# Optimization experiments

Measured on AMD Instinct MI355X. Metric: run time of the kernel, lower is better.

## Reference

```python
import jax, jax.numpy as jnp
import numpy as np

N = 16      # num_nodes
D = 128     # embedding_dim
H = 8       # num_heads
F = 512     # feedforward_dim
L = 4       # num_layers
IN = 64     # per-node input dim (joint_pos 32 + joint_vel 32)
B = 16384   # batch


def _ln(x, g, b):
    m = x.mean(-1, keepdims=True)
    v = ((x - m) ** 2).mean(-1, keepdims=True)
    return (x - m) * jax.lax.rsqrt(v + 1e-5) * g + b


def setup_inputs() -> dict:
    key = jax.random.key(0)
    ks = jax.random.split(key, 24)
    s = 0.02
    inp = {
        'joint_pos': jax.random.normal(ks[0], (B, 32), jnp.float32),
        'joint_vel': jax.random.normal(ks[1], (B, 32), jnp.float32),
        'adjacency': jax.random.randint(ks[2], (N, N), 0, 2).astype(jnp.int32),
        # per-node embedder (distinct Linear per node, stacked)
        'embed_W': jax.random.normal(ks[3], (N, IN, D), jnp.float32) * s,
        'embed_b': jnp.zeros((N, D), jnp.float32),
        'pos_emb': jax.random.normal(ks[4], (N, D), jnp.float32) * s,
        # per-layer attention params, stacked over layer dim
        'Wq': jax.random.normal(ks[5], (L, D, D), jnp.float32) * s,
        'bq': jnp.zeros((L, D), jnp.float32),
        'Wk': jax.random.normal(ks[6], (L, D, D), jnp.float32) * s,
        'bk': jnp.zeros((L, D), jnp.float32),
        'Wv': jax.random.normal(ks[7], (L, D, D), jnp.float32) * s,
        'bv': jnp.zeros((L, D), jnp.float32),
        'Wo': jax.random.normal(ks[8], (L, D, D), jnp.float32) * s,
        'bo': jnp.zeros((L, D), jnp.float32),
        'ln1_g': jnp.ones((L, D), jnp.float32),
        'ln1_b': jnp.zeros((L, D), jnp.float32),
        'ln2_g': jnp.ones((L, D), jnp.float32),
        'ln2_b': jnp.zeros((L, D), jnp.float32),
        'W1': jax.random.normal(ks[9], (L, D, F), jnp.float32) * s,
        'b1': jnp.zeros((L, F), jnp.float32),
        'W2': jax.random.normal(ks[10], (L, F, D), jnp.float32) * s,
        'b2': jnp.zeros((L, D), jnp.float32),
    }
    return inp


def reference(joint_pos, joint_vel, adjacency, embed_W, embed_b, pos_emb,
              Wq, bq, Wk, bk, Wv, bv, Wo, bo,
              ln1_g, ln1_b, ln2_g, ln2_b, W1, b1, W2, b2):
    # adjacency with forced self-loops -> additive attention mask [N, N]
    adj = adjacency.astype(bool) | jnp.eye(N, dtype=bool)
    mask = jnp.where(adj, 0.0, -jnp.inf).astype(jnp.float32)

    # every node sees the full concatenated obs (list-variant obs_node_dict)
    feats = jnp.concatenate([joint_pos, joint_vel], axis=-1)        # [B, IN]
    # distinct per-node linear embedders, batched as one einsum
    x = jnp.einsum('bi,nio->bno', feats, embed_W) + embed_b + pos_emb  # [B, N, D]

    dh = D // H
    scale = 1.0 / (dh ** 0.5)
    for l in range(L):  # BoT-Hard: mask on every layer; pre-LN
        h = _ln(x, ln1_g[l], ln1_b[l])
        q = (h @ Wq[l] + bq[l]).reshape(-1, N, H, dh)
        k = (h @ Wk[l] + bk[l]).reshape(-1, N, H, dh)
        v = (h @ Wv[l] + bv[l]).reshape(-1, N, H, dh)
        s = jnp.einsum('bnhd,bmhd->bhnm', q, k) * scale + mask       # [B, H, N, N]
        a = jax.nn.softmax(s, axis=-1)
        o = jnp.einsum('bhnm,bmhd->bnhd', a, v).reshape(-1, N, D)
        x = x + o @ Wo[l] + bo[l]
        h2 = _ln(x, ln2_g[l], ln2_b[l])
        x = x + jax.nn.relu(h2 @ W1[l] + b1[l]) @ W2[l] + b2[l]
    return x
```

## Files before the change

### kernel.cpp

```cpp
#include <hip/hip_runtime.h>
#include <stdint.h>

typedef __bf16 bf16;
typedef bf16 bf16x8 __attribute__((ext_vector_type(8)));
typedef bf16 bf16x4 __attribute__((ext_vector_type(4)));
typedef float f32x4 __attribute__((ext_vector_type(4)));
typedef uint32_t u32;
typedef uint8_t u8;

#define B_TOT 16384
#define SWG 8
#define NWGS (B_TOT / SWG)

__device__ __forceinline__ f32x4 mfma32(bf16x8 a, bf16x8 b, f32x4 c) {
  return __builtin_amdgcn_mfma_f32_16x16x32_bf16(a, b, c, 0, 0, 0);
}
__device__ __forceinline__ bf16x8 zero8() {
  bf16x8 v;
#pragma unroll
  for (int j = 0; j < 8; j++) v[j] = (bf16)0.f;
  return v;
}

__device__ __forceinline__ void lds_fence() {
  __builtin_amdgcn_sched_barrier(0);
  asm volatile("s_waitcnt lgkmcnt(0)" ::: "memory");
  __builtin_amdgcn_sched_barrier(0);
}

__device__ __forceinline__ void bar_lg() {
  __builtin_amdgcn_sched_barrier(0);
  asm volatile("s_waitcnt lgkmcnt(0)" ::: "memory");
  __builtin_amdgcn_s_barrier();
  __builtin_amdgcn_sched_barrier(0);
}
__device__ __forceinline__ void bar_v0() {
  __builtin_amdgcn_sched_barrier(0);
  asm volatile("s_waitcnt vmcnt(0) lgkmcnt(0)" ::: "memory");
  __builtin_amdgcn_s_barrier();
  __builtin_amdgcn_sched_barrier(0);
}
__device__ __forceinline__ void bar_v2() {
  __builtin_amdgcn_sched_barrier(0);
  asm volatile("s_waitcnt vmcnt(2) lgkmcnt(0)" ::: "memory");
  __builtin_amdgcn_s_barrier();
  __builtin_amdgcn_sched_barrier(0);
}

__device__ __forceinline__ void stage16(const u8* __restrict__ src, int rowstride, int colbase,
                                        u8* dst, int tid) {
  __builtin_amdgcn_sched_barrier(0);
#pragma unroll
  for (int rr = 0; rr < 2; ++rr) {
    u32 o = (u32)(rr * 512 + tid) * 16u;
    u32 row = o >> 7, cb = o & 0x7Fu;
    const u8* s = src + (size_t)row * (size_t)rowstride + (size_t)colbase
                      + (size_t)(cb ^ ((row & 7u) << 4));
    __builtin_amdgcn_global_load_lds((const __attribute__((address_space(1))) u32*)s,
                                     (__attribute__((address_space(3))) u32*)(dst + o),
                                     16, 0, 0);
  }
}

__device__ __forceinline__ void st_row(u8* base, int row, int col, bf16 v) {
  *(bf16*)(base + (u32)(row * 256) + (u32)((2 * col) ^ ((row & 7) << 4))) = v;
}

__device__ __forceinline__ void loadA_rm(const u8* R, int g, int c, bf16x8 a[2][4]) {
  const u32 sw = (u32)(c & 7) << 4;
#pragma unroll
  for (int mt = 0; mt < 2; ++mt)
#pragma unroll
    for (int ks = 0; ks < 4; ++ks)
      a[mt][ks] = *(const bf16x8*)(R + (u32)((mt * 16 + c) * 256)
                                     + (((u32)(ks * 64 + g * 16)) ^ sw));
}

__device__ __forceinline__ void gemm_half(const u8* Wb, int khalf, const bf16x8 a[2][4],
                                          f32x4 acc[2][4], int nh, int g, int c) {
  const u32 sw = (u32)(c & 7) << 4;
#pragma unroll
  for (int ksl = 0; ksl < 2; ++ksl) {
    int ks = khalf * 2 + ksl;
#pragma unroll
    for (int nt = 0; nt < 4; ++nt) {
      bf16x8 b = *(const bf16x8*)(Wb + (u32)((nh * 64 + nt * 16 + c) * 128)
                                     + (((u32)(ksl * 64 + g * 16)) ^ sw));
      acc[0][nt] = mfma32(a[0][ks], b, acc[0][nt]);
      acc[1][nt] = mfma32(a[1][ks], b, acc[1][nt]);
    }
  }
}

template <bool RELU>
__device__ __forceinline__ void epi_rm(const f32x4 acc[2][4], const float* __restrict__ bias,
                                       u8* Rdst, int nh, int g, int c) {
#pragma unroll
  for (int nt = 0; nt < 4; ++nt) {
    int col = nh * 64 + nt * 16 + c;
    float bb = bias[col];
#pragma unroll
    for (int mt = 0; mt < 2; ++mt)
#pragma unroll
      for (int r = 0; r < 4; ++r) {
        float v = acc[mt][nt][r] + bb;
        if (RELU) v = fmaxf(v, 0.f);
        st_row(Rdst, mt * 16 + 4 * g + r, col, (bf16)v);
      }
  }
}

__device__ __forceinline__ void ln_part(const f32x4 x[2][4], float sS[2][4], float sS2[2][4]) {
#pragma unroll
  for (int mt = 0; mt < 2; ++mt) {
    f32x4 a = {0.f, 0.f, 0.f, 0.f}, b = {0.f, 0.f, 0.f, 0.f};
#pragma unroll
    for (int nt = 0; nt < 4; ++nt) { a += x[mt][nt]; b += x[mt][nt] * x[mt][nt]; }
#pragma unroll
    for (int r = 0; r < 4; ++r) {
      float s = a[r], s2 = b[r];
#pragma unroll
      for (int off = 1; off < 16; off <<= 1) { s += __shfl_xor(s, off); s2 += __shfl_xor(s2, off); }
      sS[mt][r] = s; sS2[mt][r] = s2;
    }
  }
}

__global__ void __launch_bounds__(512, 2)
bot_main(const int* __restrict__ adj,
         const float* __restrict__ embB, const float* __restrict__ posE,
         const float* __restrict__ pbq, const float* __restrict__ pbk,
         const float* __restrict__ pbv, const float* __restrict__ pbo,
         const float* __restrict__ l1g, const float* __restrict__ l1b,
         const float* __restrict__ l2g, const float* __restrict__ l2b,
         const float* __restrict__ pb1, const float* __restrict__ pb2,
         const bf16* __restrict__ feats, const bf16* __restrict__ embWT,
         const bf16* __restrict__ wqT, const bf16* __restrict__ wkT,
         const bf16* __restrict__ wvT, const bf16* __restrict__ woT,
         const bf16* __restrict__ w1T, const bf16* __restrict__ w2T,
         float* __restrict__ out) {
  __shared__ u8 smem[163840];
  const int tid = threadIdx.x;
  const int w = tid >> 6, lane = tid & 63, g = lane >> 4, c = lane & 15;
  const int p = w >> 1, nh = w & 1;
  const int S0 = blockIdx.x * SWG;
  const u32 sw = (u32)(c & 7) << 4;

  u8* pairb = smem + p * 24576;
  u8* RA = pairb;
  u8* Rq = pairb + 8192;
  u8* Rk = pairb + 16384;
  u8* WB0 = smem + 98304;
  u8* WB1 = smem + 114688;
  u8* WB2 = smem + 131072;
  u8* WB3 = smem + 147456;
  float* scr = (float*)Rk;

  float maskr[4];
#pragma unroll
  for (int r = 0; r < 4; ++r) {
    int n = 4 * g + r;
    maskr[r] = (adj[n * 16 + c] != 0 || n == c) ? 0.f : -1e9f;
  }

  {
    float* x0 = (float*)smem;
    f32x4 ea[16] = {};
    bf16x8 af[2];
#pragma unroll
    for (int ks = 0; ks < 2; ++ks)
      af[ks] = *(const bf16x8*)(feats + (size_t)(S0 + (c & 7)) * 64 + ks * 32 + g * 8);
#pragma unroll
    for (int nt = 0; nt < 16; ++nt) {
#pragma unroll
      for (int ks = 0; ks < 2; ++ks) {
        bf16x8 bw = *(const bf16x8*)(embWT + (size_t)(w * 256 + nt * 16 + c) * 64 + ks * 32 + g * 8);
        ea[nt] = mfma32(af[ks], bw, ea[nt]);
      }
    }
    if (g < 2) {
#pragma unroll
      for (int nt = 0; nt < 16; ++nt)
#pragma unroll
        for (int r = 0; r < 4; ++r)
          x0[(4 * g + r) * 2048 + w * 256 + nt * 16 + c] = ea[nt][r];
    }
  }
  __syncthreads();

  f32x4 x[2][4];
  {
    const float* x0 = (const float*)smem;
#pragma unroll
    for (int nt = 0; nt < 4; ++nt)
#pragma unroll
      for (int r = 0; r < 4; ++r) {
        int n = 4 * g + r, d = nh * 64 + nt * 16 + c;
        float eb = embB[n * 128 + d] + posE[n * 128 + d];
#pragma unroll
        for (int mt = 0; mt < 2; ++mt)
          x[mt][nt][r] = x0[(2 * p + mt) * 2048 + n * 128 + d] + eb;
      }
  }
  __syncthreads();

  bf16x8 Ah[2][4], Ah2[2][4], Au[2][4];

#pragma unroll 1
  for (int l = 0; l < 4; ++l) {
    const u8* Wq_l = (const u8*)(wqT + (size_t)l * 16384);
    const u8* Wk_l = (const u8*)(wkT + (size_t)l * 16384);
    const u8* Wv_l = (const u8*)(wvT + (size_t)l * 16384);
    const u8* Wo_l = (const u8*)(woT + (size_t)l * 16384);
    const u8* W1_l = (const u8*)(w1T + (size_t)l * 65536);
    const u8* W2_l = (const u8*)(w2T + (size_t)l * 65536);

    float sS[2][4], sS2[2][4], mean[2][4], rstd[2][4];

    ln_part(x, sS, sS2);
    if (c == 0) {
#pragma unroll
      for (int mt = 0; mt < 2; ++mt)
#pragma unroll
        for (int r = 0; r < 4; ++r) {
          int row = mt * 16 + 4 * g + r;
          scr[(row * 2 + nh) * 2 + 0] = sS[mt][r];
          scr[(row * 2 + nh) * 2 + 1] = sS2[mt][r];
        }
    }
    stage16(Wq_l, 256, 0, WB0, tid);
    bar_lg();

#pragma unroll
    for (int mt = 0; mt < 2; ++mt)
#pragma unroll
      for (int r = 0; r < 4; ++r) {
        int row = mt * 16 + 4 * g + r;
        float s = sS[mt][r] + scr[(row * 2 + (1 - nh)) * 2 + 0];
        float s2 = sS2[mt][r] + scr[(row * 2 + (1 - nh)) * 2 + 1];
        float mu = s * (1.f / 128.f);
        float va = s2 * (1.f / 128.f) - mu * mu;
        mean[mt][r] = mu; rstd[mt][r] = rsqrtf(va + 1e-5f);
      }
#pragma unroll
    for (int nt = 0; nt < 4; ++nt) {
      int col = nh * 64 + nt * 16 + c;
      float gg = l1g[l * 128 + col], bb = l1b[l * 128 + col];
#pragma unroll
      for (int mt = 0; mt < 2; ++mt)
#pragma unroll
        for (int r = 0; r < 4; ++r)
          st_row(RA, mt * 16 + 4 * g + r, col,
                 (bf16)((x[mt][nt][r] - mean[mt][r]) * rstd[mt][r] * gg + bb));
    }
    stage16(Wq_l, 256, 128, WB1, tid);
    bar_v2();

    f32x4 acc[2][4];
    loadA_rm(RA, g, c, Ah);
#pragma unroll
    for (int mt = 0; mt < 2; ++mt)
#pragma unroll
      for (int nt = 0; nt < 4; ++nt) acc[mt][nt] = (f32x4){0.f, 0.f, 0.f, 0.f};
    gemm_half(WB0, 0, Ah, acc, nh, g, c);
    stage16(Wk_l, 256, 0, WB2, tid);
    bar_v2();

    gemm_half(WB1, 1, Ah, acc, nh, g, c);
    epi_rm<false>(acc, pbq + l * 128, Rq, nh, g, c);
    stage16(Wk_l, 256, 128, WB3, tid);
    bar_v2();

#pragma unroll
    for (int mt = 0; mt < 2; ++mt)
#pragma unroll
      for (int nt = 0; nt < 4; ++nt) acc[mt][nt] = (f32x4){0.f, 0.f, 0.f, 0.f};
    gemm_half(WB2, 0, Ah, acc, nh, g, c);
    stage16(Wv_l, 256, 0, WB0, tid);
    bar_v2();

    gemm_half(WB3, 1, Ah, acc, nh, g, c);
    epi_rm<false>(acc, pbk + l * 128, Rk, nh, g, c);
    stage16(Wv_l, 256, 128, WB1, tid);
    bar_v2();

#pragma unroll
    for (int mt = 0; mt < 2; ++mt)
#pragma unroll
      for (int nt = 0; nt < 4; ++nt) acc[mt][nt] = (f32x4){0.f, 0.f, 0.f, 0.f};
    gemm_half(WB0, 0, Ah, acc, nh, g, c);
    bar_v0();

    gemm_half(WB1, 1, Ah, acc, nh, g, c);
#pragma unroll
    for (int nt = 0; nt < 4; ++nt) {
      int col = nh * 64 + nt * 16 + c;
      float bb = pbv[l * 128 + col];
#pragma unroll
      for (int mt = 0; mt < 2; ++mt) {
        bf16x4 pk;
#pragma unroll
        for (int r = 0; r < 4; ++r) pk[r] = (bf16)(acc[mt][nt][r] + bb);
        *(bf16x4*)(RA + mt * 4096 + col * 32 + g * 8) = pk;
      }
    }
    stage16(Wo_l, 256, 0, WB2, tid);
    bar_lg();

    {
      const f32x4 zz = {0.f, 0.f, 0.f, 0.f};
#pragma unroll 1
      for (int hh = 0; hh < 4; ++hh) {
        const int gh = nh * 4 + hh;
        bf16x8 qf[2], kf[2];
#pragma unroll
        for (int mt = 0; mt < 2; ++mt) {
          if (g < 2) {
            qf[mt] = *(const bf16x8*)(Rq + (u32)((mt * 16 + c) * 256)
                                         + (((u32)(gh * 32 + g * 16)) ^ sw));
            kf[mt] = *(const bf16x8*)(Rk + (u32)((mt * 16 + c) * 256)
                                         + (((u32)(gh * 32 + g * 16)) ^ sw));
          } else { qf[mt] = zero8(); kf[mt] = zero8(); }
        }
        f32x4 sc[2];
        sc[0] = mfma32(qf[0], kf[0], zz);
        sc[1] = mfma32(qf[1], kf[1], zz);
        float pr[2][4], mx[2][4], sm[2][4];
#pragma unroll
        for (int mt = 0; mt < 2; ++mt)
#pragma unroll
          for (int r = 0; r < 4; ++r) { pr[mt][r] = sc[mt][r] * 0.25f + maskr[r]; mx[mt][r] = pr[mt][r]; }
#pragma unroll
        for (int off = 1; off < 16; off <<= 1)
#pragma unroll
          for (int mt = 0; mt < 2; ++mt)
#pragma unroll
            for (int r = 0; r < 4; ++r) mx[mt][r] = fmaxf(mx[mt][r], __shfl_xor(mx[mt][r], off));
#pragma unroll
        for (int mt = 0; mt < 2; ++mt)
#pragma unroll
          for (int r = 0; r < 4; ++r) { pr[mt][r] = __expf(pr[mt][r] - mx[mt][r]); sm[mt][r] = pr[mt][r]; }
#pragma unroll
        for (int off = 1; off < 16; off <<= 1)
#pragma unroll
          for (int mt = 0; mt < 2; ++mt)
#pragma unroll
            for (int r = 0; r < 4; ++r) sm[mt][r] += __shfl_xor(sm[mt][r], off);
#pragma unroll
        for (int mt = 0; mt < 2; ++mt)
#pragma unroll
          for (int r = 0; r < 4; ++r)
            st_row(Rq, mt * 16 + 4 * g + r, gh * 16 + c,
                   (bf16)(pr[mt][r] * __fdividef(1.f, sm[mt][r])));
        lds_fence();
        bf16x8 pa[2], vf[2];
#pragma unroll
        for (int mt = 0; mt < 2; ++mt) {
          if (g < 2) {
            pa[mt] = *(const bf16x8*)(Rq + (u32)((mt * 16 + c) * 256)
                                         + (((u32)(gh * 32 + g * 16)) ^ sw));
            vf[mt] = *(const bf16x8*)(RA + mt * 4096 + gh * 512 + c * 32 + g * 16);
          } else { pa[mt] = zero8(); vf[mt] = zero8(); }
        }
        f32x4 oo[2];
        oo[0] = mfma32(pa[0], vf[0], zz);
        oo[1] = mfma32(pa[1], vf[1], zz);
#pragma unroll
        for (int mt = 0; mt < 2; ++mt)
#pragma unroll
          for (int r = 0; r < 4; ++r)
            st_row(Rq, mt * 16 + 4 * g + r, gh * 16 + c, (bf16)oo[mt][r]);
      }
    }
    stage16(Wo_l, 256, 128, WB3, tid);
    bar_v2();

    loadA_rm(Rq, g, c, Ah);
    gemm_half(WB2, 0, Ah, x, nh, g, c);
    bar_v0();

    gemm_half(WB3, 1, Ah, x, nh, g, c);
#pragma unroll
    for (int nt = 0; nt < 4; ++nt) {
      float bb = pbo[l * 128 + nh * 64 + nt * 16 + c];
#pragma unroll
      for (int mt = 0; mt < 2; ++mt)
#pragma unroll
        for (int r = 0; r < 4; ++r) x[mt][nt][r] += bb;
    }
    ln_part(x, sS, sS2);
    if (c == 0) {
#pragma unroll
      for (int mt = 0; mt < 2; ++mt)
#pragma unroll
        for (int r = 0; r < 4; ++r) {
          int row = mt * 16 + 4 * g + r;
          scr[(row * 2 + nh) * 2 + 0] = sS[mt][r];
          scr[(row * 2 + nh) * 2 + 1] = sS2[mt][r];
        }
    }
    stage16(W1_l, 256, 0, WB0, tid);
    bar_lg();

#pragma unroll
    for (int mt = 0; mt < 2; ++mt)
#pragma unroll
      for (int r = 0; r < 4; ++r) {
        int row = mt * 16 + 4 * g + r;
        float s = sS[mt][r] + scr[(row * 2 + (1 - nh)) * 2 + 0];
        float s2 = sS2[mt][r] + scr[(row * 2 + (1 - nh)) * 2 + 1];
        float mu = s * (1.f / 128.f);
        float va = s2 * (1.f / 128.f) - mu * mu;
        mean[mt][r] = mu; rstd[mt][r] = rsqrtf(va + 1e-5f);
      }
#pragma unroll
    for (int nt = 0; nt < 4; ++nt) {
      int col = nh * 64 + nt * 16 + c;
      float gg = l2g[l * 128 + col], bb = l2b[l * 128 + col];
#pragma unroll
      for (int mt = 0; mt < 2; ++mt)
#pragma unroll
        for (int r = 0; r < 4; ++r)
          st_row(RA, mt * 16 + 4 * g + r, col,
                 (bf16)((x[mt][nt][r] - mean[mt][r]) * rstd[mt][r] * gg + bb));
    }
    stage16(W1_l, 256, 128, WB1, tid);
    bar_v2();

#pragma unroll 1
    for (int fc = 0; fc < 4; ++fc) {
      f32x4 uacc[2][4];
#pragma unroll
      for (int mt = 0; mt < 2; ++mt)
#pragma unroll
        for (int nt = 0; nt < 4; ++nt) uacc[mt][nt] = (f32x4){0.f, 0.f, 0.f, 0.f};
      if (fc == 0) loadA_rm(RA, g, c, Ah2);
      gemm_half(WB0, 0, Ah2, uacc, nh, g, c);
      stage16(W2_l, 1024, fc * 256, WB2, tid);
      bar_v2();
      gemm_half(WB1, 1, Ah2, uacc, nh, g, c);
      epi_rm<true>(uacc, pb1 + l * 512 + fc * 128, Rq, nh, g, c);
      stage16(W2_l, 1024, fc * 256 + 128, WB3, tid);
      bar_v2();
      loadA_rm(Rq, g, c, Au);
      gemm_half(WB2, 0, Au, x, nh, g, c);
      if (fc < 3) { stage16(W1_l + (fc + 1) * 32768, 256, 0, WB0, tid); bar_v2(); }
      else bar_v0();
      gemm_half(WB3, 1, Au, x, nh, g, c);
      if (fc < 3) { stage16(W1_l + (fc + 1) * 32768, 256, 128, WB1, tid); bar_v2(); }
      else {
#pragma unroll
        for (int nt = 0; nt < 4; ++nt) {
          float bb = pb2[l * 128 + nh * 64 + nt * 16 + c];
#pragma unroll
          for (int mt = 0; mt < 2; ++mt)
#pragma unroll
            for (int r = 0; r < 4; ++r) x[mt][nt][r] += bb;
        }
        bar_lg();
      }
    }
  }

#pragma unroll
  for (int nt = 0; nt < 4; ++nt) {
    int col = nh * 64 + nt * 16 + c;
#pragma unroll
    for (int mt = 0; mt < 2; ++mt)
      *(f32x4*)(pairb + mt * 8192 + col * 64 + g * 16) = x[mt][nt];
  }
  bar_lg();
  {
    const int smp = S0 + 2 * p + nh;
    const u8* src = pairb + nh * 8192;
#pragma unroll
    for (int it = 0; it < 8; ++it) {
      int n = it * 2 + (lane >> 5);
      int slot = lane & 31;
      f32x4 v;
#pragma unroll
      for (int e = 0; e < 4; ++e)
        v[e] = *(const float*)(src + (u32)((slot * 4 + e) * 64 + n * 4));
      *(f32x4*)(out + (size_t)smp * 2048 + n * 128 + slot * 4) = v;
    }
  }
}

__global__ void prep_feats_k(const float* __restrict__ pos, const float* __restrict__ vel,
                             bf16* __restrict__ feats) {
  int i = blockIdx.x * 256 + threadIdx.x;
  if (i >= B_TOT * 64) return;
  int b = i >> 6, k = i & 63;
  float v = (k < 32) ? pos[b * 32 + k] : vel[b * 32 + (k - 32)];
  feats[i] = (bf16)v;
}

__global__ void prep_tr_k(const float* __restrict__ src, bf16* __restrict__ dst,
                          int R, int C, int total) {
  int i = blockIdx.x * 256 + threadIdx.x;
  if (i >= total) return;
  int rc = R * C;
  int m = i / rc, rem = i % rc;
  int cc = rem / R, rr = rem % R;
  dst[i] = (bf16)src[(size_t)m * rc + rr * C + cc];
}

extern "C" void kernel_launch(void* const* d_in, const int* in_sizes, int n_in,
                              void* d_out, int out_size, void* d_ws, size_t ws_size,
                              hipStream_t stream) {
  const float* jp  = (const float*)d_in[0];
  const float* jv  = (const float*)d_in[1];
  const int*   adj = (const int*)d_in[2];
  const float* eW  = (const float*)d_in[3];
  const float* eB  = (const float*)d_in[4];
  const float* pE  = (const float*)d_in[5];
  const float* Wq  = (const float*)d_in[6];  const float* bq = (const float*)d_in[7];
  const float* Wk  = (const float*)d_in[8];  const float* bk = (const float*)d_in[9];
  const float* Wv  = (const float*)d_in[10]; const float* bv = (const float*)d_in[11];
  const float* Wo  = (const float*)d_in[12]; const float* bo = (const float*)d_in[13];
  const float* g1  = (const float*)d_in[14]; const float* be1 = (const float*)d_in[15];
  const float* g2  = (const float*)d_in[16]; const float* be2 = (const float*)d_in[17];
  const float* W1  = (const float*)d_in[18]; const float* b1 = (const float*)d_in[19];
  const float* W2  = (const float*)d_in[20]; const float* b2 = (const float*)d_in[21];

  bf16* ws    = (bf16*)d_ws;
  bf16* feats = ws;
  bf16* embWT = ws + 1048576;
  bf16* wqT   = embWT + 131072;
  bf16* wkT   = wqT + 65536;
  bf16* wvT   = wkT + 65536;
  bf16* woT   = wvT + 65536;
  bf16* w1T   = woT + 65536;
  bf16* w2T   = w1T + 262144;

  prep_feats_k<<<(B_TOT * 64 + 255) / 256, 256, 0, stream>>>(jp, jv, feats);
  prep_tr_k<<<512, 256, 0, stream>>>(eW, embWT, 64, 128, 131072);
  prep_tr_k<<<256, 256, 0, stream>>>(Wq, wqT, 128, 128, 65536);
  prep_tr_k<<<256, 256, 0, stream>>>(Wk, wkT, 128, 128, 65536);
  prep_tr_k<<<256, 256, 0, stream>>>(Wv, wvT, 128, 128, 65536);
  prep_tr_k<<<256, 256, 0, stream>>>(Wo, woT, 128, 128, 65536);
  prep_tr_k<<<1024, 256, 0, stream>>>(W1, w1T, 128, 512, 262144);
  prep_tr_k<<<1024, 256, 0, stream>>>(W2, w2T, 512, 128, 262144);

  bot_main<<<NWGS, 512, 0, stream>>>(adj, eB, pE, bq, bk, bv, bo,
                                     g1, be1, g2, be2, b1, b2,
                                     feats, embWT, wqT, wkT, wvT, woT, w1T, w2T,
                                     (float*)d_out);
}
```

Measured before the change: 1.159 ms.

## Compute attention transposed and pass P/V/O fragments through register shuffles

Attention scores are now computed transposed (K·Qᵀ), so the softmax reduction runs across lanes with two xor-shuffles plus an in-register max/sum instead of a 16-lane butterfly. Probabilities, V fragments and outputs are repacked to bf16 and redistributed into MFMA operand layout with __shfl, which removes the LDS round trip and the lgkm fence between softmax and the PV product. The head loop is fully unrolled. The LDS swizzle is widened from 3 to 4 row bits to cut bank conflicts. The cost is more cross-lane shuffles and more register pressure under a 512-thread, 2-block launch bound.

Result: faster. 1.047 ms (-9.7%).

```diff
diff --git a/kernel.cpp b/kernel.cpp
--- a/kernel.cpp
+++ b/kernel.cpp
@@ -20,12 +20,6 @@
 #pragma unroll
   for (int j = 0; j < 8; j++) v[j] = (bf16)0.f;
   return v;
-}
-
-__device__ __forceinline__ void lds_fence() {
-  __builtin_amdgcn_sched_barrier(0);
-  asm volatile("s_waitcnt lgkmcnt(0)" ::: "memory");
-  __builtin_amdgcn_sched_barrier(0);
 }
 
 __device__ __forceinline__ void bar_lg() {
@@ -63,11 +57,11 @@
 }
 
 __device__ __forceinline__ void st_row(u8* base, int row, int col, bf16 v) {
-  *(bf16*)(base + (u32)(row * 256) + (u32)((2 * col) ^ ((row & 7) << 4))) = v;
+  *(bf16*)(base + (u32)(row * 256) + (u32)((2 * col) ^ ((row & 15) << 4))) = v;
 }
 
 __device__ __forceinline__ void loadA_rm(const u8* R, int g, int c, bf16x8 a[2][4]) {
-  const u32 sw = (u32)(c & 7) << 4;
+  const u32 sw = (u32)c << 4;
 #pragma unroll
   for (int mt = 0; mt < 2; ++mt)
 #pragma unroll
@@ -108,6 +102,27 @@
         st_row(Rdst, mt * 16 + 4 * g + r, col, (bf16)v);
       }
   }
+}
+
+__device__ __forceinline__ void pack4(const f32x4 v, u32& w0, u32& w1) {
+  union { bf16 h[2]; u32 u; } t0, t1;
+  t0.h[0] = (bf16)v[0]; t0.h[1] = (bf16)v[1];
+  t1.h[0] = (bf16)v[2]; t1.h[1] = (bf16)v[3];
+  w0 = t0.u; w1 = t1.u;
+}
+
+__device__ __forceinline__ bf16x8 Rfrag(u32 w0, u32 w1, int g, int c) {
+  int s0 = 32 * g + c;
+  int s1 = 32 * g + 16 + c;
+  u32 a0 = (u32)__shfl((int)w0, s0);
+  u32 a1 = (u32)__shfl((int)w1, s0);
+  u32 a2 = (u32)__shfl((int)w0, s1);
+  u32 a3 = (u32)__shfl((int)w1, s1);
+  union { u32 u[4]; bf16x8 v; } r;
+  bool ok = (g < 2);
+  r.u[0] = ok ? a0 : 0u; r.u[1] = ok ? a1 : 0u;
+  r.u[2] = ok ? a2 : 0u; r.u[3] = ok ? a3 : 0u;
+  return r.v;
 }
 
 __device__ __forceinline__ void ln_part(const f32x4 x[2][4], float sS[2][4], float sS2[2][4]) {
@@ -144,7 +159,6 @@
   const int w = tid >> 6, lane = tid & 63, g = lane >> 4, c = lane & 15;
   const int p = w >> 1, nh = w & 1;
   const int S0 = blockIdx.x * SWG;
-  const u32 sw = (u32)(c & 7) << 4;
 
   u8* pairb = smem + p * 24576;
   u8* RA = pairb;
@@ -156,11 +170,11 @@
   u8* WB3 = smem + 147456;
   float* scr = (float*)Rk;
 
-  float maskr[4];
+  float maskT[4];
 #pragma unroll
   for (int r = 0; r < 4; ++r) {
-    int n = 4 * g + r;
-    maskr[r] = (adj[n * 16 + c] != 0 || n == c) ? 0.f : -1e9f;
+    int m = 4 * g + r;
+    maskT[r] = (adj[c * 16 + m] != 0 || c == m) ? 0.f : -1e9f;
   }
 
   {
@@ -291,17 +305,18 @@
     gemm_half(WB0, 0, Ah, acc, nh, g, c);
     bar_v0();
 
+    bf16x8 Vf[2][4];
     gemm_half(WB1, 1, Ah, acc, nh, g, c);
 #pragma unroll
     for (int nt = 0; nt < 4; ++nt) {
-      int col = nh * 64 + nt * 16 + c;
-      float bb = pbv[l * 128 + col];
+      float bb = pbv[l * 128 + nh * 64 + nt * 16 + c];
 #pragma unroll
       for (int mt = 0; mt < 2; ++mt) {
-        bf16x4 pk;
-#pragma unroll
-        for (int r = 0; r < 4; ++r) pk[r] = (bf16)(acc[mt][nt][r] + bb);
-        *(bf16x4*)(RA + mt * 4096 + col * 32 + g * 8) = pk;
+        f32x4 v;
+#pragma unroll
+        for (int r = 0; r < 4; ++r) v[r] = acc[mt][nt][r] + bb;
+        u32 w0, w1; pack4(v, w0, w1);
+        Vf[mt][nt] = Rfrag(w0, w1, g, c);
       }
     }
     stage16(Wo_l, 256, 0, WB2, tid);
@@ -309,7 +324,8 @@
 
     {
       const f32x4 zz = {0.f, 0.f, 0.f, 0.f};
-#pragma unroll 1
+      const u32 swa = (u32)c << 4;
+#pragma unroll
       for (int hh = 0; hh < 4; ++hh) {
         const int gh = nh * 4 + hh;
         bf16x8 qf[2], kf[2];
@@ -317,59 +333,38 @@
         for (int mt = 0; mt < 2; ++mt) {
           if (g < 2) {
             qf[mt] = *(const bf16x8*)(Rq + (u32)((mt * 16 + c) * 256)
-                                         + (((u32)(gh * 32 + g * 16)) ^ sw));
+                                         + (((u32)(gh * 32 + g * 16)) ^ swa));
             kf[mt] = *(const bf16x8*)(Rk + (u32)((mt * 16 + c) * 256)
-                                         + (((u32)(gh * 32 + g * 16)) ^ sw));
+                                         + (((u32)(gh * 32 + g * 16)) ^ swa));
           } else { qf[mt] = zero8(); kf[mt] = zero8(); }
         }
-        f32x4 sc[2];
-        sc[0] = mfma32(qf[0], kf[0], zz);
-        sc[1] = mfma32(qf[1], kf[1], zz);
-        float pr[2][4], mx[2][4], sm[2][4];
-#pragma unroll
-        for (int mt = 0; mt < 2; ++mt)
-#pragma unroll
-          for (int r = 0; r < 4; ++r) { pr[mt][r] = sc[mt][r] * 0.25f + maskr[r]; mx[mt][r] = pr[mt][r]; }
-#pragma unroll
-        for (int off = 1; off < 16; off <<= 1)
-#pragma unroll
-          for (int mt = 0; mt < 2; ++mt)
-#pragma unroll
-            for (int r = 0; r < 4; ++r) mx[mt][r] = fmaxf(mx[mt][r], __shfl_xor(mx[mt][r], off));
-#pragma unroll
-        for (int mt = 0; mt < 2; ++mt)
-#pragma unroll
-          for (int r = 0; r < 4; ++r) { pr[mt][r] = __expf(pr[mt][r] - mx[mt][r]); sm[mt][r] = pr[mt][r]; }
-#pragma unroll
-        for (int off = 1; off < 16; off <<= 1)
-#pragma unroll
-          for (int mt = 0; mt < 2; ++mt)
-#pragma unroll
-            for (int r = 0; r < 4; ++r) sm[mt][r] += __shfl_xor(sm[mt][r], off);
-#pragma unroll
-        for (int mt = 0; mt < 2; ++mt)
-#pragma unroll
-          for (int r = 0; r < 4; ++r)
-            st_row(Rq, mt * 16 + 4 * g + r, gh * 16 + c,
-                   (bf16)(pr[mt][r] * __fdividef(1.f, sm[mt][r])));
-        lds_fence();
-        bf16x8 pa[2], vf[2];
 #pragma unroll
         for (int mt = 0; mt < 2; ++mt) {
-          if (g < 2) {
-            pa[mt] = *(const bf16x8*)(Rq + (u32)((mt * 16 + c) * 256)
-                                         + (((u32)(gh * 32 + g * 16)) ^ sw));
-            vf[mt] = *(const bf16x8*)(RA + mt * 4096 + gh * 512 + c * 32 + g * 16);
-          } else { pa[mt] = zero8(); vf[mt] = zero8(); }
+          f32x4 st = mfma32(kf[mt], qf[mt], zz);
+          float pr[4];
+#pragma unroll
+          for (int r = 0; r < 4; ++r) pr[r] = st[r] * 0.25f + maskT[r];
+          float mx = fmaxf(fmaxf(pr[0], pr[1]), fmaxf(pr[2], pr[3]));
+          mx = fmaxf(mx, __shfl_xor(mx, 16));
+          mx = fmaxf(mx, __shfl_xor(mx, 32));
+          float sm = 0.f;
+#pragma unroll
+          for (int r = 0; r < 4; ++r) { pr[r] = __expf(pr[r] - mx); sm += pr[r]; }
+          sm += __shfl_xor(sm, 16);
+          sm += __shfl_xor(sm, 32);
+          float pinv = __fdividef(1.f, sm);
+          f32x4 pv;
+#pragma unroll
+          for (int r = 0; r < 4; ++r) pv[r] = pr[r] * pinv;
+          u32 w0, w1; pack4(pv, w0, w1);
+          bf16x8 Pf = Rfrag(w0, w1, g, c);
+          f32x4 oo = mfma32(Vf[mt][hh], Pf, zz);
+          pack4(oo, w0, w1);
+          bf16x8 Of = Rfrag(w0, w1, g, c);
+          if (g < 2)
+            *(bf16x8*)(Rq + (u32)((mt * 16 + c) * 256)
+                          + (((u32)(gh * 32 + g * 16)) ^ swa)) = Of;
         }
-        f32x4 oo[2];
-        oo[0] = mfma32(pa[0], vf[0], zz);
-        oo[1] = mfma32(pa[1], vf[1], zz);
-#pragma unroll
-        for (int mt = 0; mt < 2; ++mt)
-#pragma unroll
-          for (int r = 0; r < 4; ++r)
-            st_row(Rq, mt * 16 + 4 * g + r, gh * 16 + c, (bf16)oo[mt][r]);
       }
     }
     stage16(Wo_l, 256, 128, WB3, tid);
```
